# Optimization experiments

Hardware: AMD Instinct MI355X
Metric: run time of the kernel (lower is better)

Reference implementation:

```python
import jax, jax.numpy as jnp
import numpy as np

LEVELS = 256

def _bipolar(key, shape):
    # torchhd MAP hypervectors are random +-1
    return jnp.where(jax.random.bernoulli(key, 0.5, shape), 1.0, -1.0).astype(jnp.float32)

def setup_inputs() -> dict:
    key = jax.random.key(0)
    k1, k2, k3 = jax.random.split(key, 3)
    x = jax.random.uniform(k1, (16, 28, 28), dtype=jnp.float32)  # pixel intensities in [0,1]
    position_weight = _bipolar(k2, (784, 10000))   # Random embedding: one hv per pixel position
    value_weight = _bipolar(k3, (LEVELS, 10000))   # Level embedding table
    return {"x": x, "position_weight": position_weight, "value_weight": value_weight}

def reference(x, position_weight, value_weight):
    b = x.shape[0]
    xf = x.reshape(b, -1)                                   # (B, P) flatten
    levels = value_weight.shape[0]
    # torchhd Level: quantize value in [0,1] to nearest level index
    idx = jnp.clip(jnp.round(xf * (levels - 1)), 0, levels - 1).astype(jnp.int32)
    # gather level hvs, bind (elementwise multiply) with position hvs: (B, P, D)
    bound = value_weight[idx] * position_weight[None, :, :]
    s = bound.sum(axis=-2)                                  # multiset bundle -> (B, D)
    one = jnp.asarray(1.0, s.dtype)
    return jnp.where(s > 0, one, -one)
```

## Files before the change

### kernel.cpp

```cpp
#include <hip/hip_runtime.h>
#include <stdint.h>

constexpr int KD = 10000;
constexpr int KP = 784;
constexpr int KB = 16;
constexpr int KL = 256;
constexpr int KW = 320;
constexpr int KNWG = 80;
constexpr int KROWS = KP + KL;


__global__ __launch_bounds__(256) void pack_kernel(const float* __restrict__ pos,
                                                   const float* __restrict__ val,
                                                   uint32_t* __restrict__ posb,
                                                   uint32_t* __restrict__ valb) {
    int tid = blockIdx.x * 256 + threadIdx.x;
    int r = tid / KW;
    int W = tid - r * KW;
    const float* src = (r < KP) ? pos : val;
    int rr = (r < KP) ? r : r - KP;
    uint32_t word = 0;
    const float4* s4 = (const float4*)(src + (size_t)rr * KD + W * 32);
    if (W < 312) {
        #pragma unroll
        for (int j = 0; j < 8; ++j) {
            float4 f = s4[j];
            uint32_t s = (__float_as_uint(f.x) >> 31)
                       | ((__float_as_uint(f.y) >> 31) << 1)
                       | ((__float_as_uint(f.z) >> 31) << 2)
                       | ((__float_as_uint(f.w) >> 31) << 3);
            word |= s << (4 * j);
        }
    } else if (W == 312) {
        #pragma unroll
        for (int j = 0; j < 4; ++j) {
            float4 f = s4[j];
            uint32_t s = (__float_as_uint(f.x) >> 31)
                       | ((__float_as_uint(f.y) >> 31) << 1)
                       | ((__float_as_uint(f.z) >> 31) << 2)
                       | ((__float_as_uint(f.w) >> 31) << 3);
            word |= s << (4 * j);
        }
    }
    int wg = W >> 2, w = W & 3;
    if (r < KP) posb[((size_t)wg * KP + rr) * 4 + w] = word;
    else        valb[((size_t)wg * KL + rr) * 4 + w] = word;
}

__global__ __launch_bounds__(64) void accum_kernel(const uint32_t* __restrict__ posb,
                                                   const uint32_t* __restrict__ valb,
                                                   const float* __restrict__ x,
                                                   float* __restrict__ out) {
    __shared__ int sidx[KP];
    __shared__ uint32_t red[8][16][5];
    int wg = blockIdx.x;
    int b  = blockIdx.y;
    int t  = threadIdx.x;

    for (int p = t; p < KP; p += 64) {
        float v = x[b * KP + p] * 255.0f;
        float r = fminf(fmaxf(rintf(v), 0.0f), 255.0f);
        sidx[p] = (int)r * 16;
    }
    __syncthreads();

    int w = t & 3, g = t >> 2;
    const uint32_t* pb = posb + (size_t)wg * KP * 4 + w;
    const char*     vb = (const char*)(valb + (size_t)wg * KL * 4 + w);
    uint32_t c0 = 0, c1 = 0, c2 = 0, c3 = 0, c4 = 0, c5 = 0;
    #pragma unroll 7
    for (int i = 0; i < 49; ++i) {
        int p = i * 16 + g;
        uint32_t xp = pb[p * 4];
        uint32_t xv = *(const uint32_t*)(vb + sidx[p]);
        uint32_t carry = xp ^ xv, tt;
        tt = c0 & carry; c0 ^= carry; carry = tt;
        tt = c1 & carry; c1 ^= carry; carry = tt;
        tt = c2 & carry; c2 ^= carry; carry = tt;
        tt = c3 & carry; c3 ^= carry; carry = tt;
        tt = c4 & carry; c4 ^= carry; carry = tt;
        c5 ^= carry;
    }
    #pragma unroll
    for (int k = 0; k < 8; ++k) {
        uint32_t vk = ((c0 >> k) & 0x01010101u)
                    | (((c1 >> k) & 0x01010101u) << 1)
                    | (((c2 >> k) & 0x01010101u) << 2)
                    | (((c3 >> k) & 0x01010101u) << 3)
                    | (((c4 >> k) & 0x01010101u) << 4)
                    | (((c5 >> k) & 0x01010101u) << 5);
        red[k][g][w] = vk;
    }
    __syncthreads();

    if (t < 32) {
        int rw = t & 3, rk = t >> 2;
        uint32_t lo = 0, hi = 0;
        #pragma unroll
        for (int gg = 0; gg < 16; ++gg) {
            uint32_t v = red[rk][gg][rw];
            lo += v & 0x00FF00FFu;
            hi += (v >> 8) & 0x00FF00FFu;
        }
        int c_0  = (int)(lo & 0xFFFFu);
        int c_16 = (int)(lo >> 16);
        int c_8  = (int)(hi & 0xFFFFu);
        int c_24 = (int)(hi >> 16);
        int dbase = wg * 128 + rw * 32 + rk;
        float* ob = out + (size_t)b * KD;
        if (dbase      < KD) ob[dbase]      = (c_0  < 392) ? 1.0f : -1.0f;
        if (dbase + 8  < KD) ob[dbase + 8]  = (c_8  < 392) ? 1.0f : -1.0f;
        if (dbase + 16 < KD) ob[dbase + 16] = (c_16 < 392) ? 1.0f : -1.0f;
        if (dbase + 24 < KD) ob[dbase + 24] = (c_24 < 392) ? 1.0f : -1.0f;
    }
}

extern "C" void kernel_launch(void* const* d_in, const int* in_sizes, int n_in,
                              void* d_out, int out_size, void* d_ws, size_t ws_size,
                              hipStream_t stream) {
    const float* x   = (const float*)d_in[0];
    const float* pos = (const float*)d_in[1];
    const float* val = (const float*)d_in[2];
    float* out = (float*)d_out;

    char* ws = (char*)d_ws;
    uint32_t* posb = (uint32_t*)ws;
    uint32_t* valb = (uint32_t*)(ws + (size_t)KNWG * KP * 4 * sizeof(uint32_t));

    pack_kernel<<<1300, 256, 0, stream>>>(pos, val, posb, valb);
    accum_kernel<<<dim3(79, KB), 64, 0, stream>>>(posb, valb, x, out);
}
```

Baseline: 94.61 us.

## Pack signs with wavefront ballot and split accumulation across four waves

The pack kernel now gives each block one row: each wave reads contiguous floats one per lane, which coalesces the loads, and uses __ballot to form 64-bit sign masks in place of per-thread strided float4 loads. The accumulation kernel grows from 64 to 256 threads, with each wave handling a quarter of the positions. Each wave keeps a 4-bit bit-sliced counter, and the partial counts are combined in shared memory, so there are four times more waves per tile to hide gather latency. The cost is a larger reduction in shared memory and more sidx work spread over the wider block.

```diff
diff --git a/kernel.cpp b/kernel.cpp
--- a/kernel.cpp
+++ b/kernel.cpp
@@ -5,91 +5,88 @@
 constexpr int KP = 784;
 constexpr int KB = 16;
 constexpr int KL = 256;
-constexpr int KW = 320;
-constexpr int KNWG = 80;
 constexpr int KROWS = KP + KL;
+constexpr int KCHUNK = 157;
 
 
 __global__ __launch_bounds__(256) void pack_kernel(const float* __restrict__ pos,
                                                    const float* __restrict__ val,
                                                    uint32_t* __restrict__ posb,
                                                    uint32_t* __restrict__ valb) {
-    int tid = blockIdx.x * 256 + threadIdx.x;
-    int r = tid / KW;
-    int W = tid - r * KW;
-    const float* src = (r < KP) ? pos : val;
-    int rr = (r < KP) ? r : r - KP;
-    uint32_t word = 0;
-    const float4* s4 = (const float4*)(src + (size_t)rr * KD + W * 32);
-    if (W < 312) {
-        #pragma unroll
-        for (int j = 0; j < 8; ++j) {
-            float4 f = s4[j];
-            uint32_t s = (__float_as_uint(f.x) >> 31)
-                       | ((__float_as_uint(f.y) >> 31) << 1)
-                       | ((__float_as_uint(f.z) >> 31) << 2)
-                       | ((__float_as_uint(f.w) >> 31) << 3);
-            word |= s << (4 * j);
-        }
-    } else if (W == 312) {
-        #pragma unroll
-        for (int j = 0; j < 4; ++j) {
-            float4 f = s4[j];
-            uint32_t s = (__float_as_uint(f.x) >> 31)
-                       | ((__float_as_uint(f.y) >> 31) << 1)
-                       | ((__float_as_uint(f.z) >> 31) << 2)
-                       | ((__float_as_uint(f.w) >> 31) << 3);
-            word |= s << (4 * j);
+    int r    = blockIdx.x;
+    int t    = threadIdx.x;
+    int lane = t & 63;
+    int sub  = t >> 6;
+
+    const float* src;
+    uint32_t* dst;
+    int rr, rowstride;
+    if (r < KP) { src = pos; dst = posb; rr = r;      rowstride = KP; }
+    else        { src = val; dst = valb; rr = r - KP; rowstride = KL; }
+    const float* srow = src + (size_t)rr * KD;
+
+    int cbeg = sub * 40;
+    int cend = min(cbeg + 40, KCHUNK);
+    #pragma unroll 4
+    for (int c = cbeg; c < cend; ++c) {
+        int d = c * 64 + lane;
+        uint32_t sgn = 0;
+        if (d < KD) sgn = __float_as_uint(srow[d]) >> 31;
+        unsigned long long m = __ballot(sgn != 0);
+        if (lane < 2) {
+            int W = 2 * c + lane;
+            uint32_t word = (uint32_t)(m >> (32 * lane));
+            dst[((size_t)(W >> 2) * rowstride + rr) * 4 + (W & 3)] = word;
         }
     }
-    int wg = W >> 2, w = W & 3;
-    if (r < KP) posb[((size_t)wg * KP + rr) * 4 + w] = word;
-    else        valb[((size_t)wg * KL + rr) * 4 + w] = word;
+    if (sub == 3 && lane < 6) {
+        int W = 314 + lane;
+        dst[((size_t)(W >> 2) * rowstride + rr) * 4 + (W & 3)] = 0u;
+    }
 }
 
-__global__ __launch_bounds__(64) void accum_kernel(const uint32_t* __restrict__ posb,
-                                                   const uint32_t* __restrict__ valb,
-                                                   const float* __restrict__ x,
-                                                   float* __restrict__ out) {
+__global__ __launch_bounds__(256) void accum_kernel(const uint32_t* __restrict__ posb,
+                                                    const uint32_t* __restrict__ valb,
+                                                    const float* __restrict__ x,
+                                                    float* __restrict__ out) {
     __shared__ int sidx[KP];
-    __shared__ uint32_t red[8][16][5];
+    __shared__ uint32_t red[4][8][16][5];
     int wg = blockIdx.x;
     int b  = blockIdx.y;
     int t  = threadIdx.x;
 
-    for (int p = t; p < KP; p += 64) {
+    for (int p = t; p < KP; p += 256) {
         float v = x[b * KP + p] * 255.0f;
         float r = fminf(fmaxf(rintf(v), 0.0f), 255.0f);
         sidx[p] = (int)r * 16;
     }
     __syncthreads();
 
-    int w = t & 3, g = t >> 2;
+    int w = t & 3, g = (t >> 2) & 15, sub = t >> 6;
     const uint32_t* pb = posb + (size_t)wg * KP * 4 + w;
     const char*     vb = (const char*)(valb + (size_t)wg * KL * 4 + w);
-    uint32_t c0 = 0, c1 = 0, c2 = 0, c3 = 0, c4 = 0, c5 = 0;
-    #pragma unroll 7
-    for (int i = 0; i < 49; ++i) {
-        int p = i * 16 + g;
-        uint32_t xp = pb[p * 4];
-        uint32_t xv = *(const uint32_t*)(vb + sidx[p]);
-        uint32_t carry = xp ^ xv, tt;
-        tt = c0 & carry; c0 ^= carry; carry = tt;
-        tt = c1 & carry; c1 ^= carry; carry = tt;
-        tt = c2 & carry; c2 ^= carry; carry = tt;
-        tt = c3 & carry; c3 ^= carry; carry = tt;
-        tt = c4 & carry; c4 ^= carry; carry = tt;
-        c5 ^= carry;
+    uint32_t c0 = 0, c1 = 0, c2 = 0, c3 = 0;
+    #pragma unroll
+    for (int ii = 0; ii < 13; ++ii) {
+        int i = sub + ii * 4;
+        if (i < 49) {
+            int p = i * 16 + g;
+            uint32_t xp = pb[p * 4];
+            uint32_t xv = *(const uint32_t*)(vb + sidx[p]);
+            uint32_t carry = xp ^ xv, tt;
+            tt = c0 & carry; c0 ^= carry; carry = tt;
+            tt = c1 & carry; c1 ^= carry; carry = tt;
+            tt = c2 & carry; c2 ^= carry; carry = tt;
+            c3 ^= carry;
+        }
     }
     #pragma unroll
     for (int k = 0; k < 8; ++k) {
         uint32_t vk = ((c0 >> k) & 0x01010101u)
                     | (((c1 >> k) & 0x01010101u) << 1)
                     | (((c2 >> k) & 0x01010101u) << 2)
-                    | (((c3 >> k) & 0x01010101u) << 3)
-                    | (((c4 >> k) & 0x01010101u) << 4)
-                    | (((c5 >> k) & 0x01010101u) << 5);
-        red[k][g][w] = vk;
+                    | (((c3 >> k) & 0x01010101u) << 3);
+        red[sub][k][g][w] = vk;
     }
     __syncthreads();
 
@@ -97,10 +94,13 @@
         int rw = t & 3, rk = t >> 2;
         uint32_t lo = 0, hi = 0;
         #pragma unroll
-        for (int gg = 0; gg < 16; ++gg) {
-            uint32_t v = red[rk][gg][rw];
-            lo += v & 0x00FF00FFu;
-            hi += (v >> 8) & 0x00FF00FFu;
+        for (int ss = 0; ss < 4; ++ss) {
+            #pragma unroll
+            for (int gg = 0; gg < 16; ++gg) {
+                uint32_t v = red[ss][rk][gg][rw];
+                lo += v & 0x00FF00FFu;
+                hi += (v >> 8) & 0x00FF00FFu;
+            }
         }
         int c_0  = (int)(lo & 0xFFFFu);
         int c_16 = (int)(lo >> 16);
@@ -125,8 +125,8 @@
 
     char* ws = (char*)d_ws;
     uint32_t* posb = (uint32_t*)ws;
-    uint32_t* valb = (uint32_t*)(ws + (size_t)KNWG * KP * 4 * sizeof(uint32_t));
+    uint32_t* valb = (uint32_t*)(ws + (size_t)80 * KP * 4 * sizeof(uint32_t));
 
-    pack_kernel<<<1300, 256, 0, stream>>>(pos, val, posb, valb);
-    accum_kernel<<<dim3(79, KB), 64, 0, stream>>>(posb, valb, x, out);
+    pack_kernel<<<KROWS, 256, 0, stream>>>(pos, val, posb, valb);
+    accum_kernel<<<dim3(79, KB), 256, 0, stream>>>(posb, valb, x, out);
 }
```

Result: slower. 107.1 us (+13.2%).
